# Performance work log

Hardware: AMD Instinct MI355X
Metric: run time of the kernel (lower is better)

Reference implementation:

```python
import jax, jax.numpy as jnp
import numpy as np

DILS = (1, 2, 4, 8)
BN_EPS = 1e-5
NORM_EPS = 1e-12


def _affinity(xn, d):
    """Cosine affinity of each pixel with its 8 dilated 3x3 neighbors.
    xn: L2-normalized features [B,C,H,W]. Zero padding => out-of-bounds affinity = 0.
    Returns [B,8,H,W] with channels in unfold (row-major window) order, center removed,
    clamped at 0 (matches `affinity[affinity < 0] = 0`).
    """
    B, C, H, W = xn.shape
    p = jnp.pad(xn, ((0, 0), (0, 0), (d, d), (d, d)))
    chans = []
    for i in range(3):
        for j in range(3):
            if i == 1 and j == 1:
                continue  # skip center (index win_h*win_w//2 == 4)
            nb = p[:, :, i * d:i * d + H, j * d:j * d + W]
            chans.append(jnp.sum(nb * xn, axis=1))
    return jnp.maximum(jnp.stack(chans, axis=1), 0.0)


def _bn_relu(x, g, b):
    # BatchNorm2d in training mode (batch statistics, biased variance), then ReLU.
    m = jnp.mean(x, axis=(0, 2, 3), keepdims=True)
    v = jnp.var(x, axis=(0, 2, 3), keepdims=True)
    y = (x - m) / jnp.sqrt(v + BN_EPS)
    return jnp.maximum(y * g[None, :, None, None] + b[None, :, None, None], 0.0)


def setup_inputs() -> dict:
    key = jax.random.key(0)
    ks = jax.random.split(key, 8)
    B, C, H, W, sfc = 4, 32, 320, 640, 32
    inp = {"x": jax.random.normal(ks[0], (B, C, H, W), dtype=jnp.float32)}
    for i in range(4):
        inp[f"w{i+1}"] = jax.random.normal(ks[1 + i], (sfc, 8), dtype=jnp.float32) * 0.1
        inp[f"g{i+1}"] = jnp.ones((sfc,), dtype=jnp.float32)
        inp[f"b{i+1}"] = jnp.zeros((sfc,), dtype=jnp.float32)
    inp["w_last"] = jax.random.normal(ks[5], (sfc, 4 * sfc, 3, 3), dtype=jnp.float32) * 0.05
    inp["g_last"] = jnp.ones((sfc,), dtype=jnp.float32)
    inp["b_last"] = jnp.zeros((sfc,), dtype=jnp.float32)
    inp["w_final"] = jax.random.normal(ks[6], (sfc, sfc), dtype=jnp.float32) * 0.1
    return inp


def reference(x, w1, g1, b1, w2, g2, b2, w3, g3, b3, w4, g4, b4,
              w_last, g_last, b_last, w_final):
    # F.normalize(x, dim=1, p=2): x / max(||x||_2, eps)
    norm = jnp.sqrt(jnp.sum(x * x, axis=1, keepdims=True))
    xn = x / jnp.maximum(norm, NORM_EPS)

    branches = ((w1, g1, b1), (w2, g2, b2), (w3, g3, b3), (w4, g4, b4))
    feats = []
    for d, (w, g, b) in zip(DILS, branches):
        a = _affinity(xn, d)                       # [B,8,H,W]
        h = jnp.einsum('bchw,oc->bohw', a, w)      # 1x1 conv, no bias
        feats.append(_bn_relu(h, g, b))            # [B,sfc,H,W]

    cat = jnp.concatenate(feats, axis=1)           # [B,4*sfc,H,W]
    h = jax.lax.conv_general_dilated(
        cat, w_last, window_strides=(1, 1), padding=((1, 1), (1, 1)),
        dimension_numbers=('NCHW', 'OIHW', 'NCHW'))
    h = _bn_relu(h, g_last, b_last)
    out = jnp.einsum('bchw,oc->bohw', h, w_final)  # final 1x1 conv, no bias
    return out
```

## Files before the change

kernel.cpp:

```cpp
#include <hip/hip_runtime.h>
#include <math.h>

#define BB 4
#define CC0 32
#define HH 320
#define WW 640
#define HWp (HH*WW)
#define CHWp (CC0*HWp)
#define NCH (BB*HWp)
#define CCAT 128

#define WT_OFF  ((size_t)0)
#define ST_OFF  ((size_t)36864)
#define SC_OFF  ((size_t)37184)
#define CATF_OFF ((size_t)37504)

typedef unsigned short ushort_t;
typedef __attribute__((ext_vector_type(8)))  short  short8;
typedef __attribute__((ext_vector_type(16))) float  float16v;

static __device__ __forceinline__ float bf2f(ushort_t u) {
  unsigned x = ((unsigned)u) << 16;
  float f; __builtin_memcpy(&f, &x, 4); return f;
}
static __device__ __forceinline__ ushort_t f2bf(float f) {
  unsigned x; __builtin_memcpy(&x, &f, 4);
  unsigned r = (x + 0x7fffu + ((x >> 16) & 1u)) >> 16;
  return (ushort_t)r;
}
static __device__ __forceinline__ unsigned pack2(float a, float b) {
  return (unsigned)f2bf(a) | ((unsigned)f2bf(b) << 16);
}
static __device__ __forceinline__ void unpack8(uint4 u, float* f) {
  f[0] = bf2f((ushort_t)(u.x & 0xffff)); f[1] = bf2f((ushort_t)(u.x >> 16));
  f[2] = bf2f((ushort_t)(u.y & 0xffff)); f[3] = bf2f((ushort_t)(u.y >> 16));
  f[4] = bf2f((ushort_t)(u.z & 0xffff)); f[5] = bf2f((ushort_t)(u.z >> 16));
  f[6] = bf2f((ushort_t)(u.w & 0xffff)); f[7] = bf2f((ushort_t)(u.w >> 16));
}

__global__ __launch_bounds__(256) void k_normalize(const float* __restrict__ x,
                                                   ushort_t* __restrict__ xnb) {
  int pix = blockIdx.x * 256 + threadIdx.x;
  int b   = blockIdx.y;
  const float* xp = x + (size_t)b * CHWp + pix;
  float v[32];
  float s = 0.f;
  #pragma unroll
  for (int c = 0; c < 32; ++c) { v[c] = xp[(size_t)c * HWp]; s += v[c] * v[c]; }
  float inv = 1.f / fmaxf(sqrtf(s), 1e-12f);
  uint4* op = (uint4*)(xnb + ((size_t)b * HWp + pix) * 32);
  #pragma unroll
  for (int q = 0; q < 4; ++q) {
    uint4 u;
    u.x = pack2(v[q*8+0]*inv, v[q*8+1]*inv);
    u.y = pack2(v[q*8+2]*inv, v[q*8+3]*inv);
    u.z = pack2(v[q*8+4]*inv, v[q*8+5]*inv);
    u.w = pack2(v[q*8+6]*inv, v[q*8+7]*inv);
    op[q] = u;
  }
}

__global__ __launch_bounds__(256) void k_branch(const ushort_t* __restrict__ xnb,
                                                const float* __restrict__ w0,
                                                const float* __restrict__ w1,
                                                const float* __restrict__ w2,
                                                const float* __restrict__ w3,
                                                ushort_t* __restrict__ cat) {
  int z = blockIdx.z;
  int d = 1 << z;
  const float* w = (z == 0) ? w0 : (z == 1) ? w1 : (z == 2) ? w2 : w3;
  int pix = blockIdx.x * 256 + threadIdx.x;
  int b   = blockIdx.y;
  int y = pix / WW;
  int x = pix - y * WW;

  int   ofs[8];
  float msk[8];
  {
    int kk = 0;
    #pragma unroll
    for (int i = 0; i < 3; ++i)
      #pragma unroll
      for (int j = 0; j < 3; ++j) {
        if (i == 1 && j == 1) continue;
        int dy = (i - 1) * d, dx = (j - 1) * d;
        bool ok = ((unsigned)(y + dy) < (unsigned)HH) && ((unsigned)(x + dx) < (unsigned)WW);
        ofs[kk] = ok ? (dy * WW + dx) : 0;
        msk[kk] = ok ? 1.f : 0.f;
        ++kk;
      }
  }

  const ushort_t* cp0 = xnb + ((size_t)b * HWp + pix) * 32;
  const uint4* cv = (const uint4*)cp0;
  float cen[32];
  {
    uint4 c0 = cv[0], c1 = cv[1], c2 = cv[2], c3 = cv[3];
    unpack8(c0, cen); unpack8(c1, cen + 8); unpack8(c2, cen + 16); unpack8(c3, cen + 24);
  }

  float acc[8] = {0.f,0.f,0.f,0.f,0.f,0.f,0.f,0.f};
  #pragma unroll
  for (int k = 0; k < 8; ++k) {
    const uint4* np = (const uint4*)(cp0 + (ptrdiff_t)ofs[k] * 32);
    uint4 n0 = np[0], n1 = np[1], n2 = np[2], n3 = np[3];
    float nb[32];
    unpack8(n0, nb); unpack8(n1, nb + 8); unpack8(n2, nb + 16); unpack8(n3, nb + 24);
    float a = 0.f;
    #pragma unroll
    for (int c = 0; c < 32; ++c) a = fmaf(cen[c], nb[c], a);
    acc[k] = a;
  }
  float a[8];
  #pragma unroll
  for (int k = 0; k < 8; ++k) a[k] = fmaxf(acc[k], 0.f) * msk[k];

  float r[32];
  #pragma unroll
  for (int o = 0; o < 32; ++o) {
    float hv = 0.f;
    #pragma unroll
    for (int k = 0; k < 8; ++k) hv = fmaf(a[k], w[o * 8 + k], hv);
    r[o] = hv;
  }
  uint4* cp = (uint4*)(cat + ((size_t)b * HWp + pix) * 128 + z * 32);
  #pragma unroll
  for (int q = 0; q < 4; ++q) {
    uint4 u;
    u.x = pack2(r[q*8+0], r[q*8+1]);
    u.y = pack2(r[q*8+2], r[q*8+3]);
    u.z = pack2(r[q*8+4], r[q*8+5]);
    u.w = pack2(r[q*8+6], r[q*8+7]);
    cp[q] = u;
  }
}

__global__ __launch_bounds__(256) void k_stats_cat(const ushort_t* __restrict__ cat,
                                                   float* __restrict__ g_s,
                                                   float* __restrict__ g_q) {
  int t = threadIdx.x;
  int ch = (t & 63) * 2;
  size_t pix0 = (size_t)blockIdx.x * 1024 + (t >> 6);
  float s0=0.f,q0=0.f,s1=0.f,q1=0.f;
  for (int j = 0; j < 256; ++j) {
    unsigned u = *(const unsigned*)&cat[(pix0 + (size_t)j*4) * 128 + ch];
    float v0 = bf2f((ushort_t)(u & 0xffff));
    float v1 = bf2f((ushort_t)(u >> 16));
    s0 += v0; q0 += v0*v0; s1 += v1; q1 += v1*v1;
  }
  __shared__ float ls0[256], lq0[256], ls1[256], lq1[256];
  ls0[t]=s0; lq0[t]=q0; ls1[t]=s1; lq1[t]=q1;
  __syncthreads();
  if (t < 64) {
    float a0=0,b0=0,a1=0,b1=0;
    #pragma unroll
    for (int k = 0; k < 4; ++k) {
      a0 += ls0[t + 64*k]; b0 += lq0[t + 64*k];
      a1 += ls1[t + 64*k]; b1 += lq1[t + 64*k];
    }
    atomicAdd(g_s + ch, a0);     atomicAdd(g_q + ch, b0);
    atomicAdd(g_s + ch + 1, a1); atomicAdd(g_q + ch + 1, b1);
  }
}

__global__ __launch_bounds__(256) void k_stats_f32(const float* __restrict__ t,
                                                   float* __restrict__ g_s,
                                                   float* __restrict__ g_q) {
  int c = blockIdx.y, b = blockIdx.z;
  size_t base = ((size_t)b * 32 + c) * HWp + (size_t)blockIdx.x * 8192;
  const float* p = t + base + threadIdx.x;
  float s = 0.f, q = 0.f;
  #pragma unroll
  for (int j = 0; j < 32; ++j) { float v = p[j * 256]; s += v; q += v * v; }
  #pragma unroll
  for (int off = 32; off > 0; off >>= 1) {
    s += __shfl_down(s, off, 64);
    q += __shfl_down(q, off, 64);
  }
  __shared__ float ls[4], lq[4];
  int lane = threadIdx.x & 63, wid = threadIdx.x >> 6;
  if (lane == 0) { ls[wid] = s; lq[wid] = q; }
  __syncthreads();
  if (threadIdx.x == 0) {
    float ts=0, tq=0;
    #pragma unroll
    for (int i = 0; i < 4; ++i) { ts += ls[i]; tq += lq[i]; }
    atomicAdd(g_s + c, ts); atomicAdd(g_q + c, tq);
  }
}

__global__ void k_bnfin(const float* __restrict__ s, const float* __restrict__ q,
                        const float* g0, const float* g1, const float* g2, const float* g3,
                        const float* b0, const float* b1, const float* b2, const float* b3,
                        float* __restrict__ scale, float* __restrict__ shift, int Cc) {
  int c = threadIdx.x;
  if (c >= Cc) return;
  const float* g; const float* bb; int ci;
  if (Cc == 128) {
    int z = c >> 5; ci = c & 31;
    g  = (z == 0) ? g0 : (z == 1) ? g1 : (z == 2) ? g2 : g3;
    bb = (z == 0) ? b0 : (z == 1) ? b1 : (z == 2) ? b2 : b3;
  } else { g = g0; bb = b0; ci = c; }
  float mean = s[c] / (float)NCH;
  float var  = q[c] / (float)NCH - mean * mean;
  float inv  = 1.f / sqrtf(var + 1e-5f);
  float scv  = g[ci] * inv;
  scale[c] = scv;
  shift[c] = bb[ci] - mean * scv;
}

__global__ void k_wt(const float* __restrict__ wl, ushort_t* __restrict__ wbf) {
  int idx = blockIdx.x * 256 + threadIdx.x;
  if (idx >= 9 * 8 * 64 * 8) return;
  int j = idx & 7;
  int l = (idx >> 3) & 63;
  int tc = idx >> 9;
  int t = tc >> 3, cg = tc & 7;
  int o = l & 31;
  int ch = cg * 16 + ((l >> 5) << 3) + j;
  wbf[idx] = f2bf(wl[(o * 128 + ch) * 9 + t]);
}

#define SROWS 6
#define SCOLS 34
#define CHPAD 72
__global__ __launch_bounds__(256, 4) void k_conv(const ushort_t* __restrict__ cat,
                                                 const ushort_t* __restrict__ wbf,
                                                 const float* __restrict__ scale,
                                                 const float* __restrict__ shift,
                                                 float* __restrict__ out) {
  __shared__ __align__(16) ushort_t s_in[SROWS * SCOLS * CHPAD];
  int lane = threadIdx.x;
  int w    = threadIdx.y;
  int tid  = w * 64 + lane;
  int gx0 = blockIdx.x * 32, gy0 = blockIdx.y * 4;
  int b = blockIdx.z;
  size_t bHW = (size_t)b * HWp;

  const short8* wfr = (const short8*)wbf;
  float16v acc = {};

  int site0 = tid >> 3;
  int chp   = tid & 7;

  #pragma unroll
  for (int r = 0; r < 2; ++r) {
    int chb = r * 64 + chp * 8;
    float4 sc0 = *(const float4*)&scale[chb];
    float4 sc1 = *(const float4*)&scale[chb + 4];
    float4 sh0 = *(const float4*)&shift[chb];
    float4 sh1 = *(const float4*)&shift[chb + 4];
    float scl[8] = {sc0.x,sc0.y,sc0.z,sc0.w,sc1.x,sc1.y,sc1.z,sc1.w};
    float shf[8] = {sh0.x,sh0.y,sh0.z,sh0.w,sh1.x,sh1.y,sh1.z,sh1.w};

    if (r) __syncthreads();
    for (int s = site0; s < SROWS * SCOLS; s += 32) {
      int row = s / SCOLS, col = s - row * SCOLS;
      int gy = gy0 - 1 + row, gx = gx0 - 1 + col;
      uint4 u = {0u,0u,0u,0u};
      if ((unsigned)gy < (unsigned)HH && (unsigned)gx < (unsigned)WW) {
        uint4 raw = *(const uint4*)&cat[(bHW + (size_t)gy * WW + gx) * 128 + chb];
        unsigned rw[4] = {raw.x, raw.y, raw.z, raw.w};
        unsigned pk[4];
        #pragma unroll
        for (int q = 0; q < 4; ++q) {
          float v0 = fmaxf(fmaf(bf2f((ushort_t)(rw[q] & 0xffff)), scl[q*2],   shf[q*2]),   0.f);
          float v1 = fmaxf(fmaf(bf2f((ushort_t)(rw[q] >> 16)),    scl[q*2+1], shf[q*2+1]), 0.f);
          pk[q] = pack2(v0, v1);
        }
        u.x = pk[0]; u.y = pk[1]; u.z = pk[2]; u.w = pk[3];
      }
      *(uint4*)&s_in[(size_t)s * CHPAD + chp * 8] = u;
    }
    __syncthreads();

    int pcol = lane & 31;
    int half = lane >> 5;
    #pragma unroll
    for (int t = 0; t < 9; ++t) {
      int ky = t / 3, kx = t - ky * 3;
      int rowbase = ((w + ky) * SCOLS + pcol + kx) * CHPAD + half * 8;
      #pragma unroll
      for (int c = 0; c < 4; ++c) {
        short8 bfrag = wfr[(t * 8 + r * 4 + c) * 64 + lane];
        short8 afrag = *(const short8*)&s_in[rowbase + c * 16];
        acc = __builtin_amdgcn_mfma_f32_32x32x16_bf16(afrag, bfrag, acc, 0, 0, 0);
      }
    }
  }

  __syncthreads();
  float* epi = (float*)s_in + w * (32 * 33);
  int half = lane >> 5, mm = lane & 31;
  #pragma unroll
  for (int r16 = 0; r16 < 16; ++r16) {
    int m = (r16 & 3) + 8 * (r16 >> 2) + 4 * half;
    epi[m * 33 + mm] = acc[r16];
  }
  __syncthreads();
  size_t obase = bHW + (size_t)(gy0 + w) * WW + gx0 + mm;
  #pragma unroll
  for (int i = 0; i < 16; ++i) {
    int o = half * 16 + i;
    out[(size_t)o * HWp + obase + (size_t)b * (CHWp - HWp)] = epi[mm * 33 + o];
  }
}

__global__ __launch_bounds__(256) void k_final(const float* hin,
                                               const float* __restrict__ wf,
                                               const float* __restrict__ scale,
                                               const float* __restrict__ shift,
                                               float* out) {
  int pix = blockIdx.x * 256 + threadIdx.x;
  int b   = blockIdx.y;
  const float* hp = hin + (size_t)b * CHWp + pix;
  float v[32];
  #pragma unroll
  for (int c = 0; c < 32; ++c)
    v[c] = fmaxf(hp[(size_t)c * HWp] * scale[c] + shift[c], 0.f);
  float r[32];
  #pragma unroll
  for (int o = 0; o < 32; ++o) {
    float s = 0.f;
    #pragma unroll
    for (int c = 0; c < 32; ++c) s = fmaf(v[c], wf[o * 32 + c], s);
    r[o] = s;
  }
  float* op = out + (size_t)b * CHWp + pix;
  #pragma unroll
  for (int o = 0; o < 32; ++o) op[(size_t)o * HWp] = r[o];
}

extern "C" void kernel_launch(void* const* d_in, const int* in_sizes, int n_in,
                              void* d_out, int out_size, void* d_ws, size_t ws_size,
                              hipStream_t stream) {
  const float* x      = (const float*)d_in[0];
  const float* w1     = (const float*)d_in[1];
  const float* g1     = (const float*)d_in[2];
  const float* b1     = (const float*)d_in[3];
  const float* w2     = (const float*)d_in[4];
  const float* g2     = (const float*)d_in[5];
  const float* b2     = (const float*)d_in[6];
  const float* w3     = (const float*)d_in[7];
  const float* g3     = (const float*)d_in[8];
  const float* b3     = (const float*)d_in[9];
  const float* w4     = (const float*)d_in[10];
  const float* g4     = (const float*)d_in[11];
  const float* b4     = (const float*)d_in[12];
  const float* w_last = (const float*)d_in[13];
  const float* g_last = (const float*)d_in[14];
  const float* b_last = (const float*)d_in[15];
  const float* w_fin  = (const float*)d_in[16];

  float* ws = (float*)d_ws;
  ushort_t* wbf = (ushort_t*)(ws + WT_OFF);
  float*    st  = ws + ST_OFF;
  float*    sc  = ws + SC_OFF;
  ushort_t* cat = (ushort_t*)(ws + CATF_OFF);

  ushort_t* xnb = (ushort_t*)d_out;
  float*    xn  = (float*)d_out;

  hipMemsetAsync(st, 0, 320 * sizeof(float), stream);

  k_normalize<<<dim3(800, 4), 256, 0, stream>>>(x, xnb);
  k_branch<<<dim3(800, 4, 4), 256, 0, stream>>>(xnb, w1, w2, w3, w4, cat);
  k_stats_cat<<<800, 256, 0, stream>>>(cat, st, st + 128);
  k_bnfin<<<1, 128, 0, stream>>>(st, st + 128, g1, g2, g3, g4, b1, b2, b3, b4,
                                 sc, sc + 128, 128);
  k_wt<<<144, 256, 0, stream>>>(w_last, wbf);
  k_conv<<<dim3(20, 80, 4), dim3(64, 4), 0, stream>>>(cat, wbf, sc, sc + 128, xn);
  k_stats_f32<<<dim3(25, 32, 4), 256, 0, stream>>>(xn, st + 256, st + 288);
  k_bnfin<<<1, 128, 0, stream>>>(st + 256, st + 288, g_last, g_last, g_last, g_last,
                                 b_last, b_last, b_last, b_last, sc + 256, sc + 288, 32);
  k_final<<<dim3(800, 4), 256, 0, stream>>>(xn, w_fin, sc + 256, sc + 288, (float*)d_out);
}
```

Baseline: 649.3 us.

## Fuse four dilation branches into one kernel and vectorize elementwise kernels

The four branch launches are merged into one kernel that loads the center pixel once, loops over the four dilations, and writes the full 128-channel concat row. Block indices are swizzled, presumably for locality. Normalize and final now process two pixels per thread with float2 loads and stores. The BN statistics kernels use 16-byte loads and wider per-thread channel groups. Together these aim to cut redundant center loads and launches and to widen memory accesses, at the cost of more registers per thread.

Result: slower. 698.8 us (+7.6%).

```diff
diff --git a/kernel.cpp b/kernel.cpp
--- a/kernel.cpp
+++ b/kernel.cpp
@@ -40,126 +40,128 @@
 
 __global__ __launch_bounds__(256) void k_normalize(const float* __restrict__ x,
                                                    ushort_t* __restrict__ xnb) {
-  int pix = blockIdx.x * 256 + threadIdx.x;
-  int b   = blockIdx.y;
-  const float* xp = x + (size_t)b * CHWp + pix;
-  float v[32];
-  float s = 0.f;
-  #pragma unroll
-  for (int c = 0; c < 32; ++c) { v[c] = xp[(size_t)c * HWp]; s += v[c] * v[c]; }
-  float inv = 1.f / fmaxf(sqrtf(s), 1e-12f);
-  uint4* op = (uint4*)(xnb + ((size_t)b * HWp + pix) * 32);
+  int p2 = blockIdx.x * 256 + threadIdx.x;
+  int b  = blockIdx.y;
+  const float2* xp = (const float2*)(x + (size_t)b * CHWp) + p2;
+  float va[32], vb[32];
+  float sa = 0.f, sb = 0.f;
+  #pragma unroll
+  for (int c = 0; c < 32; ++c) {
+    float2 v = xp[c * (HWp/2)];
+    va[c] = v.x; vb[c] = v.y;
+    sa = fmaf(v.x, v.x, sa); sb = fmaf(v.y, v.y, sb);
+  }
+  float ia = 1.f / fmaxf(sqrtf(sa), 1e-12f);
+  float ib = 1.f / fmaxf(sqrtf(sb), 1e-12f);
+  uint4* op = (uint4*)(xnb + ((size_t)b * HWp + (size_t)p2 * 2) * 32);
   #pragma unroll
   for (int q = 0; q < 4; ++q) {
     uint4 u;
-    u.x = pack2(v[q*8+0]*inv, v[q*8+1]*inv);
-    u.y = pack2(v[q*8+2]*inv, v[q*8+3]*inv);
-    u.z = pack2(v[q*8+4]*inv, v[q*8+5]*inv);
-    u.w = pack2(v[q*8+6]*inv, v[q*8+7]*inv);
+    u.x = pack2(va[q*8+0]*ia, va[q*8+1]*ia);
+    u.y = pack2(va[q*8+2]*ia, va[q*8+3]*ia);
+    u.z = pack2(va[q*8+4]*ia, va[q*8+5]*ia);
+    u.w = pack2(va[q*8+6]*ia, va[q*8+7]*ia);
     op[q] = u;
   }
-}
-
-__global__ __launch_bounds__(256) void k_branch(const ushort_t* __restrict__ xnb,
-                                                const float* __restrict__ w0,
-                                                const float* __restrict__ w1,
-                                                const float* __restrict__ w2,
-                                                const float* __restrict__ w3,
-                                                ushort_t* __restrict__ cat) {
-  int z = blockIdx.z;
-  int d = 1 << z;
-  const float* w = (z == 0) ? w0 : (z == 1) ? w1 : (z == 2) ? w2 : w3;
-  int pix = blockIdx.x * 256 + threadIdx.x;
+  #pragma unroll
+  for (int q = 0; q < 4; ++q) {
+    uint4 u;
+    u.x = pack2(vb[q*8+0]*ib, vb[q*8+1]*ib);
+    u.y = pack2(vb[q*8+2]*ib, vb[q*8+3]*ib);
+    u.z = pack2(vb[q*8+4]*ib, vb[q*8+5]*ib);
+    u.w = pack2(vb[q*8+6]*ib, vb[q*8+7]*ib);
+    op[4 + q] = u;
+  }
+}
+
+__global__ __launch_bounds__(256, 4) void k_branch4(const ushort_t* __restrict__ xnb,
+                                                    const float* __restrict__ w0,
+                                                    const float* __restrict__ w1,
+                                                    const float* __restrict__ w2,
+                                                    const float* __restrict__ w3,
+                                                    ushort_t* __restrict__ cat) {
+  int bx = blockIdx.x;
+  bx = (bx & 7) * 100 + (bx >> 3);
+  int pix = bx * 256 + threadIdx.x;
   int b   = blockIdx.y;
   int y = pix / WW;
   int x = pix - y * WW;
 
-  int   ofs[8];
-  float msk[8];
-  {
-    int kk = 0;
-    #pragma unroll
-    for (int i = 0; i < 3; ++i)
-      #pragma unroll
-      for (int j = 0; j < 3; ++j) {
-        if (i == 1 && j == 1) continue;
-        int dy = (i - 1) * d, dx = (j - 1) * d;
-        bool ok = ((unsigned)(y + dy) < (unsigned)HH) && ((unsigned)(x + dx) < (unsigned)WW);
-        ofs[kk] = ok ? (dy * WW + dx) : 0;
-        msk[kk] = ok ? 1.f : 0.f;
-        ++kk;
-      }
-  }
-
   const ushort_t* cp0 = xnb + ((size_t)b * HWp + pix) * 32;
-  const uint4* cv = (const uint4*)cp0;
   float cen[32];
   {
+    const uint4* cv = (const uint4*)cp0;
     uint4 c0 = cv[0], c1 = cv[1], c2 = cv[2], c3 = cv[3];
     unpack8(c0, cen); unpack8(c1, cen + 8); unpack8(c2, cen + 16); unpack8(c3, cen + 24);
   }
-
-  float acc[8] = {0.f,0.f,0.f,0.f,0.f,0.f,0.f,0.f};
-  #pragma unroll
-  for (int k = 0; k < 8; ++k) {
-    const uint4* np = (const uint4*)(cp0 + (ptrdiff_t)ofs[k] * 32);
-    uint4 n0 = np[0], n1 = np[1], n2 = np[2], n3 = np[3];
-    float nb[32];
-    unpack8(n0, nb); unpack8(n1, nb + 8); unpack8(n2, nb + 16); unpack8(n3, nb + 24);
-    float a = 0.f;
-    #pragma unroll
-    for (int c = 0; c < 32; ++c) a = fmaf(cen[c], nb[c], a);
-    acc[k] = a;
-  }
-  float a[8];
-  #pragma unroll
-  for (int k = 0; k < 8; ++k) a[k] = fmaxf(acc[k], 0.f) * msk[k];
-
-  float r[32];
-  #pragma unroll
-  for (int o = 0; o < 32; ++o) {
-    float hv = 0.f;
-    #pragma unroll
-    for (int k = 0; k < 8; ++k) hv = fmaf(a[k], w[o * 8 + k], hv);
-    r[o] = hv;
-  }
-  uint4* cp = (uint4*)(cat + ((size_t)b * HWp + pix) * 128 + z * 32);
-  #pragma unroll
-  for (int q = 0; q < 4; ++q) {
-    uint4 u;
-    u.x = pack2(r[q*8+0], r[q*8+1]);
-    u.y = pack2(r[q*8+2], r[q*8+3]);
-    u.z = pack2(r[q*8+4], r[q*8+5]);
-    u.w = pack2(r[q*8+6], r[q*8+7]);
-    cp[q] = u;
+  uint4* cp = (uint4*)(cat + ((size_t)b * HWp + pix) * 128);
+
+  #pragma unroll 1
+  for (int z = 0; z < 4; ++z) {
+    int d = 1 << z;
+    const float* w = (z == 0) ? w0 : (z == 1) ? w1 : (z == 2) ? w2 : w3;
+    const int DY[8] = {-1,-1,-1, 0, 0, 1, 1, 1};
+    const int DX[8] = {-1, 0, 1,-1, 1,-1, 0, 1};
+    float a[8];
+    #pragma unroll
+    for (int k = 0; k < 8; ++k) {
+      int dy = DY[k] * d, dx = DX[k] * d;
+      bool ok = ((unsigned)(y + dy) < (unsigned)HH) && ((unsigned)(x + dx) < (unsigned)WW);
+      int ofs = ok ? (dy * WW + dx) : 0;
+      const uint4* np = (const uint4*)(cp0 + (ptrdiff_t)ofs * 32);
+      uint4 n0 = np[0], n1 = np[1], n2 = np[2], n3 = np[3];
+      float nb[32];
+      unpack8(n0, nb); unpack8(n1, nb + 8); unpack8(n2, nb + 16); unpack8(n3, nb + 24);
+      float acc = 0.f;
+      #pragma unroll
+      for (int c = 0; c < 32; ++c) acc = fmaf(cen[c], nb[c], acc);
+      a[k] = ok ? fmaxf(acc, 0.f) : 0.f;
+    }
+    #pragma unroll
+    for (int q = 0; q < 4; ++q) {
+      unsigned pw[4];
+      #pragma unroll
+      for (int pp = 0; pp < 4; ++pp) {
+        int o = q * 8 + pp * 2;
+        float h0 = 0.f, h1 = 0.f;
+        #pragma unroll
+        for (int k = 0; k < 8; ++k) {
+          h0 = fmaf(a[k], w[o * 8 + k], h0);
+          h1 = fmaf(a[k], w[(o + 1) * 8 + k], h1);
+        }
+        pw[pp] = pack2(h0, h1);
+      }
+      uint4 u; u.x = pw[0]; u.y = pw[1]; u.z = pw[2]; u.w = pw[3];
+      cp[z * 4 + q] = u;
+    }
   }
 }
 
 __global__ __launch_bounds__(256) void k_stats_cat(const ushort_t* __restrict__ cat,
                                                    float* __restrict__ g_s,
                                                    float* __restrict__ g_q) {
-  int t = threadIdx.x;
-  int ch = (t & 63) * 2;
-  size_t pix0 = (size_t)blockIdx.x * 1024 + (t >> 6);
-  float s0=0.f,q0=0.f,s1=0.f,q1=0.f;
-  for (int j = 0; j < 256; ++j) {
-    unsigned u = *(const unsigned*)&cat[(pix0 + (size_t)j*4) * 128 + ch];
-    float v0 = bf2f((ushort_t)(u & 0xffff));
-    float v1 = bf2f((ushort_t)(u >> 16));
-    s0 += v0; q0 += v0*v0; s1 += v1; q1 += v1*v1;
-  }
-  __shared__ float ls0[256], lq0[256], ls1[256], lq1[256];
-  ls0[t]=s0; lq0[t]=q0; ls1[t]=s1; lq1[t]=q1;
+  int t  = threadIdx.x;
+  int cg = t & 15;
+  int pr = t >> 4;
+  size_t pix0 = (size_t)blockIdx.x * 2048 + pr;
+  const uint4* base = (const uint4*)cat;
+  float s[8] = {0,0,0,0,0,0,0,0}, q[8] = {0,0,0,0,0,0,0,0};
+  for (int j = 0; j < 128; ++j) {
+    size_t pix = pix0 + (size_t)j * 16;
+    uint4 u = base[pix * 16 + cg];
+    float v[8]; unpack8(u, v);
+    #pragma unroll
+    for (int i = 0; i < 8; ++i) { s[i] += v[i]; q[i] = fmaf(v[i], v[i], q[i]); }
+  }
+  __shared__ float ls[16][128], lq[16][128];
+  #pragma unroll
+  for (int i = 0; i < 8; ++i) { ls[pr][cg*8+i] = s[i]; lq[pr][cg*8+i] = q[i]; }
   __syncthreads();
-  if (t < 64) {
-    float a0=0,b0=0,a1=0,b1=0;
-    #pragma unroll
-    for (int k = 0; k < 4; ++k) {
-      a0 += ls0[t + 64*k]; b0 += lq0[t + 64*k];
-      a1 += ls1[t + 64*k]; b1 += lq1[t + 64*k];
-    }
-    atomicAdd(g_s + ch, a0);     atomicAdd(g_q + ch, b0);
-    atomicAdd(g_s + ch + 1, a1); atomicAdd(g_q + ch + 1, b1);
+  if (t < 128) {
+    float a = 0.f, bq = 0.f;
+    #pragma unroll
+    for (int r = 0; r < 16; ++r) { a += ls[r][t]; bq += lq[r][t]; }
+    atomicAdd(g_s + t, a); atomicAdd(g_q + t, bq);
   }
 }
 
@@ -168,10 +170,15 @@
                                                    float* __restrict__ g_q) {
   int c = blockIdx.y, b = blockIdx.z;
   size_t base = ((size_t)b * 32 + c) * HWp + (size_t)blockIdx.x * 8192;
-  const float* p = t + base + threadIdx.x;
+  const float4* p = (const float4*)(t + base) + threadIdx.x;
   float s = 0.f, q = 0.f;
   #pragma unroll
-  for (int j = 0; j < 32; ++j) { float v = p[j * 256]; s += v; q += v * v; }
+  for (int j = 0; j < 8; ++j) {
+    float4 v = p[j * 256];
+    s += v.x + v.y + v.z + v.w;
+    q = fmaf(v.x, v.x, q); q = fmaf(v.y, v.y, q);
+    q = fmaf(v.z, v.z, q); q = fmaf(v.w, v.w, q);
+  }
   #pragma unroll
   for (int off = 32; off > 0; off >>= 1) {
     s += __shfl_down(s, off, 64);
@@ -182,7 +189,7 @@
   if (lane == 0) { ls[wid] = s; lq[wid] = q; }
   __syncthreads();
   if (threadIdx.x == 0) {
-    float ts=0, tq=0;
+    float ts = 0, tq = 0;
     #pragma unroll
     for (int i = 0; i < 4; ++i) { ts += ls[i]; tq += lq[i]; }
     atomicAdd(g_s + c, ts); atomicAdd(g_q + c, tq);
@@ -311,24 +318,29 @@
                                                const float* __restrict__ scale,
                                                const float* __restrict__ shift,
                                                float* out) {
-  int pix = blockIdx.x * 256 + threadIdx.x;
-  int b   = blockIdx.y;
-  const float* hp = hin + (size_t)b * CHWp + pix;
-  float v[32];
-  #pragma unroll
-  for (int c = 0; c < 32; ++c)
-    v[c] = fmaxf(hp[(size_t)c * HWp] * scale[c] + shift[c], 0.f);
-  float r[32];
+  int p2 = blockIdx.x * 256 + threadIdx.x;
+  int b  = blockIdx.y;
+  const float2* hp = (const float2*)(hin + (size_t)b * CHWp) + p2;
+  float va[32], vb[32];
+  #pragma unroll
+  for (int c = 0; c < 32; ++c) {
+    float2 v = hp[c * (HWp/2)];
+    va[c] = fmaxf(fmaf(v.x, scale[c], shift[c]), 0.f);
+    vb[c] = fmaxf(fmaf(v.y, scale[c], shift[c]), 0.f);
+  }
+  float2* op = (float2*)(out + (size_t)b * CHWp) + p2;
   #pragma unroll
   for (int o = 0; o < 32; ++o) {
-    float s = 0.f;
-    #pragma unroll
-    for (int c = 0; c < 32; ++c) s = fmaf(v[c], wf[o * 32 + c], s);
-    r[o] = s;
-  }
-  float* op = out + (size_t)b * CHWp + pix;
-  #pragma unroll
-  for (int o = 0; o < 32; ++o) op[(size_t)o * HWp] = r[o];
+    float ra = 0.f, rb = 0.f;
+    #pragma unroll
+    for (int c = 0; c < 32; ++c) {
+      float wv = wf[o * 32 + c];
+      ra = fmaf(va[c], wv, ra);
+      rb = fmaf(vb[c], wv, rb);
+    }
+    float2 rr; rr.x = ra; rr.y = rb;
+    op[o * (HWp/2)] = rr;
+  }
 }
 
 extern "C" void kernel_launch(void* const* d_in, const int* in_sizes, int n_in,
@@ -363,9 +375,9 @@
 
   hipMemsetAsync(st, 0, 320 * sizeof(float), stream);
 
-  k_normalize<<<dim3(800, 4), 256, 0, stream>>>(x, xnb);
-  k_branch<<<dim3(800, 4, 4), 256, 0, stream>>>(xnb, w1, w2, w3, w4, cat);
-  k_stats_cat<<<800, 256, 0, stream>>>(cat, st, st + 128);
+  k_normalize<<<dim3(400, 4), 256, 0, stream>>>(x, xnb);
+  k_branch4<<<dim3(800, 4), 256, 0, stream>>>(xnb, w1, w2, w3, w4, cat);
+  k_stats_cat<<<400, 256, 0, stream>>>(cat, st, st + 128);
   k_bnfin<<<1, 128, 0, stream>>>(st, st + 128, g1, g2, g3, g4, b1, b2, b3, b4,
                                  sc, sc + 128, 128);
   k_wt<<<144, 256, 0, stream>>>(w_last, wbf);
@@ -373,5 +385,5 @@
   k_stats_f32<<<dim3(25, 32, 4), 256, 0, stream>>>(xn, st + 256, st + 288);
   k_bnfin<<<1, 128, 0, stream>>>(st + 256, st + 288, g_last, g_last, g_last, g_last,
                                  b_last, b_last, b_last, b_last, sc + 256, sc + 288, 32);
-  k_final<<<dim3(800, 4), 256, 0, stream>>>(xn, w_fin, sc + 256, sc + 288, (float*)d_out);
-}
+  k_final<<<dim3(400, 4), 256, 0, stream>>>(xn, w_fin, sc + 256, sc + 288, (float*)d_out);
+}
```
